# Optimization experiments

Measured on AMD Instinct MI355X. Metric: run time of the kernel, lower is better.

The kernel has to match this reference:

```python
import jax, jax.numpy as jnp
import numpy as np

B, T, C, H = 4, 4096, 1024, 128

def setup_inputs() -> dict:
    key = jax.random.key(0)
    k1, k2, k3, k4 = jax.random.split(key, 4)
    x = jax.random.normal(k1, (B, T, C), dtype=jnp.float32)
    # nn.Linear(embed, head, bias=False): y = x @ W, store W as [C, H]
    s = 1.0 / np.sqrt(C)
    Wk = jax.random.normal(k2, (C, H), dtype=jnp.float32) * s
    Wq = jax.random.normal(k3, (C, H), dtype=jnp.float32) * s
    Wv = jax.random.normal(k4, (C, H), dtype=jnp.float32) * s
    return {"x": x, "Wk": Wk, "Wq": Wq, "Wv": Wv}

def reference(x, Wk, Wq, Wv):
    Bx, Tx, Cx = x.shape
    scale = Wk.shape[1] ** -0.5
    k = x @ Wk  # [B,T,H]
    q = x @ Wq
    v = x @ Wv
    att = jnp.einsum('bth,bsh->bts', q, k) * scale  # [B,T,T]
    causal = jnp.triu(jnp.ones((Tx, Tx), dtype=bool), k=1)
    att = jnp.where(causal, -jnp.inf, att)
    att = jax.nn.softmax(att, axis=-1)
    # dropout is identity in eval mode
    out = jnp.einsum('bts,bsh->bth', att, v)  # [B,T,H]
    return out
```

## Files before the change

### kernel.cpp

```cpp
#include <hip/hip_runtime.h>
#include <stdint.h>
#include <math.h>

#define B_ 4
#define T_ 4096
#define C_ 1024
#define H_ 128

typedef __attribute__((ext_vector_type(8))) short s16x8;
typedef __attribute__((ext_vector_type(4))) float f32x4;

__device__ __forceinline__ unsigned short f2bf(float f) {
    union { float f; unsigned u; } v; v.f = f;
    unsigned r = v.u + 0x7fffu + ((v.u >> 16) & 1u);
    return (unsigned short)(r >> 16);
}

__device__ __forceinline__ s16x8 as_frag(uint4 u) {
    union { uint4 u; s16x8 s; } v; v.u = u; return v.s;
}

#define DPP_STEP(x, ctrl, op)                                                  \
    x = op(x, __int_as_float(__builtin_amdgcn_update_dpp(                      \
               0, __float_as_int(x), ctrl, 0xF, 0xF, true)))

__device__ __forceinline__ float red16_max(float x) {
    DPP_STEP(x, 0xB1, fmaxf); DPP_STEP(x, 0x4E, fmaxf);
    DPP_STEP(x, 0x141, fmaxf); DPP_STEP(x, 0x140, fmaxf);
    return x;
}
__device__ __forceinline__ float addf(float a, float b) { return a + b; }
__device__ __forceinline__ float red16_sum(float x) {
    DPP_STEP(x, 0xB1, addf); DPP_STEP(x, 0x4E, addf);
    DPP_STEP(x, 0x141, addf); DPP_STEP(x, 0x140, addf);
    return x;
}

#define QSC (0.0883883476f * 1.4426950408f)

__global__ __launch_bounds__(256) void k_wt(const float* __restrict__ Wk,
                                            const float* __restrict__ Wq,
                                            const float* __restrict__ Wv,
                                            unsigned short* __restrict__ Wt) {
    __shared__ float tile[64][65];
    int w = blockIdx.z;
    const float* W = (w == 0) ? Wk : (w == 1) ? Wq : Wv;
    int c0 = blockIdx.x * 64, h0 = blockIdx.y * 64;
    int tid = threadIdx.x;
#pragma unroll
    for (int k = 0; k < 16; k++) {
        int idx = tid + k * 256;
        int r = idx >> 6, c = idx & 63;
        tile[r][c] = W[(size_t)(c0 + r) * H_ + h0 + c];
    }
    __syncthreads();
#pragma unroll
    for (int k = 0; k < 16; k++) {
        int idx = tid + k * 256;
        int hh = idx >> 6, cc = idx & 63;
        Wt[(size_t)(w * H_ + h0 + hh) * C_ + c0 + cc] = f2bf(tile[cc][hh]);
    }
}

__global__ __launch_bounds__(256, 2) void k_qkv(const float* __restrict__ x,
                                                const unsigned short* __restrict__ Wt,
                                                unsigned short* __restrict__ Qb,
                                                unsigned short* __restrict__ Kb,
                                                unsigned short* __restrict__ Vt) {
    __shared__ unsigned short a_lds[64 * 72];
    int tid = threadIdx.x;
    int wv = tid >> 6, lane = tid & 63, quad = lane >> 4, lo = lane & 15;
    int r0 = blockIdx.x * 64;
    int cb = blockIdx.y;
    int nt0 = wv * 3;

    f32x4 acc[3][4];
#pragma unroll
    for (int i = 0; i < 3; i++)
#pragma unroll
        for (int j = 0; j < 4; j++) acc[i][j] = (f32x4){0.f, 0.f, 0.f, 0.f};

    const int row_s = tid >> 2;
    const int seg_s = (tid & 3) * 16;
    size_t xbase = (size_t)(r0 + row_s) * C_ + seg_s;

    const unsigned short* wp[3];
#pragma unroll
    for (int nt = 0; nt < 3; nt++)
        wp[nt] = Wt + (size_t)(cb * 192 + (nt0 + nt) * 16 + lo) * C_ + quad * 8;

    auto pack_store = [&](const float4 (&f)[4]) {
        uint4 u0, u1;
        u0.x = (unsigned)f2bf(f[0].x) | ((unsigned)f2bf(f[0].y) << 16);
        u0.y = (unsigned)f2bf(f[0].z) | ((unsigned)f2bf(f[0].w) << 16);
        u0.z = (unsigned)f2bf(f[1].x) | ((unsigned)f2bf(f[1].y) << 16);
        u0.w = (unsigned)f2bf(f[1].z) | ((unsigned)f2bf(f[1].w) << 16);
        u1.x = (unsigned)f2bf(f[2].x) | ((unsigned)f2bf(f[2].y) << 16);
        u1.y = (unsigned)f2bf(f[2].z) | ((unsigned)f2bf(f[2].w) << 16);
        u1.z = (unsigned)f2bf(f[3].x) | ((unsigned)f2bf(f[3].y) << 16);
        u1.w = (unsigned)f2bf(f[3].z) | ((unsigned)f2bf(f[3].w) << 16);
        *(uint4*)&a_lds[row_s * 72 + seg_s] = u0;
        *(uint4*)&a_lds[row_s * 72 + seg_s + 8] = u1;
    };
    auto load_x = [&](float4 (&f)[4], int kc) {
        const float* xp = x + xbase + kc * 64;
#pragma unroll
        for (int j = 0; j < 4; j++) f[j] = *(const float4*)(xp + j * 4);
    };
    auto load_b = [&](s16x8 (&b)[3][2], int kc) {
#pragma unroll
        for (int nt = 0; nt < 3; nt++)
#pragma unroll
            for (int kh = 0; kh < 2; kh++)
                b[nt][kh] = *(const s16x8*)(wp[nt] + kc * 64 + kh * 32);
    };
    auto gemm = [&](const s16x8 (&b)[3][2]) {
        s16x8 af[4][2];
#pragma unroll
        for (int mt = 0; mt < 4; mt++)
#pragma unroll
            for (int kh = 0; kh < 2; kh++)
                af[mt][kh] = *(const s16x8*)&a_lds[(mt * 16 + lo) * 72 + kh * 32 + quad * 8];
#pragma unroll
        for (int nt = 0; nt < 3; nt++)
#pragma unroll
            for (int kh = 0; kh < 2; kh++)
#pragma unroll
                for (int mt = 0; mt < 4; mt++)
                    acc[nt][mt] = __builtin_amdgcn_mfma_f32_16x16x32_bf16(
                        af[mt][kh], b[nt][kh], acc[nt][mt], 0, 0, 0);
    };

    float4 xa[4], xb[4];
    s16x8 ba[3][2], bb[3][2];
    load_x(xa, 0);
    load_b(ba, 0);

    for (int kc2 = 0; kc2 < 8; kc2++) {
        int e = kc2 * 2;
        pack_store(xa);
        load_x(xb, e + 1);
        __syncthreads();
        load_b(bb, e + 1);
        gemm(ba);
        __syncthreads();
        pack_store(xb);
        if (kc2 < 7) load_x(xa, e + 2);
        __syncthreads();
        if (kc2 < 7) load_b(ba, e + 2);
        gemm(bb);
        __syncthreads();
    }

#pragma unroll
    for (int nt = 0; nt < 3; nt++) {
        int col = cb * 192 + (nt0 + nt) * 16 + lo;
        int w = col >> 7, h = col & 127;
#pragma unroll
        for (int mt = 0; mt < 4; mt++) {
            int mrow = r0 + mt * 16 + quad * 4;
            if (w == 2) {
                int b = mrow >> 12, t = mrow & 4095;
                uint2 pk;
                pk.x = (unsigned)f2bf(acc[nt][mt][0]) | ((unsigned)f2bf(acc[nt][mt][1]) << 16);
                pk.y = (unsigned)f2bf(acc[nt][mt][2]) | ((unsigned)f2bf(acc[nt][mt][3]) << 16);
                *(uint2*)(Vt + (size_t)(b * H_ + h) * T_ + t) = pk;
            } else if (w == 1) {
                unsigned short* dst = Qb + (size_t)mrow * H_ + h;
#pragma unroll
                for (int r = 0; r < 4; r++)
                    dst[(size_t)r * H_] = f2bf(acc[nt][mt][r] * QSC);
            } else {
                unsigned short* dst = Kb + (size_t)mrow * H_ + h;
#pragma unroll
                for (int r = 0; r < 4; r++)
                    dst[(size_t)r * H_] = f2bf(acc[nt][mt][r]);
            }
        }
    }
}

#define LOAD_KV(kv0)                                                            \
    do {                                                                        \
        const uint4* kg = (const uint4*)(Kb + (size_t)(batch * T_ + (kv0) + srow_k) * H_); \
        pk0 = kg[sseg_k + 0]; pk1 = kg[sseg_k + 1];                             \
        pk2 = kg[sseg_k + 2]; pk3 = kg[sseg_k + 3];                             \
        const uint4* vg = (const uint4*)(Vt + (size_t)(batch * H_ + srow_v) * T_ + (kv0)); \
        pv0 = vg[sseg_v + 0]; pv1 = vg[sseg_v + 1];                             \
        pv2 = vg[sseg_v + 2]; pv3 = vg[sseg_v + 3];                             \
    } while (0)

template <int NSPLIT>
__global__ __launch_bounds__(256, 3) void k_attn(const unsigned short* __restrict__ Qb,
                                                 const unsigned short* __restrict__ Kb,
                                                 const unsigned short* __restrict__ Vt,
                                                 float* __restrict__ Opart,
                                                 float* __restrict__ Mpart,
                                                 float* __restrict__ Lpart,
                                                 float* __restrict__ out) {
    __shared__ uint4 kbuf[64 * 16];
    __shared__ uint4 vbuf[128 * 8];
    __shared__ unsigned short pbuf[4][16 * 64];

    int tid = threadIdx.x;
    int wv = tid >> 6, lane = tid & 63, quad = lane >> 4, lo = lane & 15;

    int id = blockIdx.x;
    int qt = 63 - id / (4 * NSPLIT);
    int rem = id % (4 * NSPLIT);
    int batch = rem / NSPLIT;
    int split = rem % NSPLIT;
    int m0 = qt * 64 + wv * 16;

    s16x8 qf[4];
    size_t qrow = (size_t)(batch * T_ + m0 + lo) * H_;
#pragma unroll
    for (int ks = 0; ks < 4; ks++)
        qf[ks] = *(const s16x8*)(Qb + qrow + ks * 32 + quad * 8);

    f32x4 acc_o[8];
#pragma unroll
    for (int o = 0; o < 8; o++) acc_o[o] = (f32x4){0.f, 0.f, 0.f, 0.f};
    float m_i[4], l_i[4];
#pragma unroll
    for (int r = 0; r < 4; r++) { m_i[r] = -INFINITY; l_i[r] = 0.f; }

    const int srow_k = tid >> 2, sseg_k = (tid & 3) * 4;
    const int srow_v = tid >> 1, sseg_v = (tid & 1) * 4;

    uint4 pk0, pk1, pk2, pk3, pv0, pv1, pv2, pv3;
    LOAD_KV(split * 64);

    for (int t = split; t <= qt; t += NSPLIT) {
        int kv0 = t * 64;
        kbuf[srow_k * 16 + ((sseg_k + 0) ^ (srow_k & 15))] = pk0;
        kbuf[srow_k * 16 + ((sseg_k + 1) ^ (srow_k & 15))] = pk1;
        kbuf[srow_k * 16 + ((sseg_k + 2) ^ (srow_k & 15))] = pk2;
        kbuf[srow_k * 16 + ((sseg_k + 3) ^ (srow_k & 15))] = pk3;
        vbuf[srow_v * 8 + ((sseg_v + 0) ^ (srow_v & 7))] = pv0;
        vbuf[srow_v * 8 + ((sseg_v + 1) ^ (srow_v & 7))] = pv1;
        vbuf[srow_v * 8 + ((sseg_v + 2) ^ (srow_v & 7))] = pv2;
        vbuf[srow_v * 8 + ((sseg_v + 3) ^ (srow_v & 7))] = pv3;
        __syncthreads();
        if (t + NSPLIT <= qt) LOAD_KV((t + NSPLIT) * 64);

        f32x4 s_acc[4];
#pragma unroll
        for (int nt = 0; nt < 4; nt++) s_acc[nt] = (f32x4){0.f, 0.f, 0.f, 0.f};
#pragma unroll
        for (int ks = 0; ks < 4; ks++) {
#pragma unroll
            for (int nt = 0; nt < 4; nt++) {
                s16x8 kf = as_frag(kbuf[(nt * 16 + lo) * 16 + ((ks * 4 + quad) ^ lo)]);
                s_acc[nt] = __builtin_amdgcn_mfma_f32_16x16x32_bf16(qf[ks], kf, s_acc[nt], 0, 0, 0);
            }
        }

        float p[4][4];
        bool diag = (t == qt);
#pragma unroll
        for (int nt = 0; nt < 4; nt++)
#pragma unroll
            for (int r = 0; r < 4; r++) {
                float sv = s_acc[nt][r];
                if (diag) {
                    int colg = kv0 + nt * 16 + lo;
                    int rowg = m0 + quad * 4 + r;
                    if (colg > rowg) sv = -INFINITY;
                }
                p[nt][r] = sv;
            }
        float mnew[4], alpha[4];
#pragma unroll
        for (int r = 0; r < 4; r++) {
            float mx = fmaxf(fmaxf(p[0][r], p[1][r]), fmaxf(p[2][r], p[3][r]));
            mx = red16_max(mx);
            mnew[r] = fmaxf(m_i[r], mx);
            alpha[r] = exp2f(m_i[r] - mnew[r]);
            m_i[r] = mnew[r];
        }
        float rs[4] = {0.f, 0.f, 0.f, 0.f};
#pragma unroll
        for (int nt = 0; nt < 4; nt++)
#pragma unroll
            for (int r = 0; r < 4; r++) {
                float pv = exp2f(p[nt][r] - mnew[r]);
                p[nt][r] = pv;
                rs[r] += pv;
            }
#pragma unroll
        for (int r = 0; r < 4; r++) {
            l_i[r] = l_i[r] * alpha[r] + red16_sum(rs[r]);
        }
#pragma unroll
        for (int o = 0; o < 8; o++)
#pragma unroll
            for (int r = 0; r < 4; r++) acc_o[o][r] *= alpha[r];

        unsigned short* pb = pbuf[wv];
#pragma unroll
        for (int nt = 0; nt < 4; nt++)
#pragma unroll
            for (int r = 0; r < 4; r++) {
                int prow = quad * 4 + r;
                int col = nt * 16 + lo;
                int seg = col >> 3, off = col & 7;
                pb[prow * 64 + ((seg ^ (prow & 7)) << 3) + off] = f2bf(p[nt][r]);
            }
        s16x8 pf[2];
#pragma unroll
        for (int kss = 0; kss < 2; kss++) {
            int seg = kss * 4 + quad;
            pf[kss] = *(const s16x8*)&pb[lo * 64 + ((seg ^ (lo & 7)) << 3)];
        }

#pragma unroll
        for (int kss = 0; kss < 2; kss++)
#pragma unroll
            for (int o = 0; o < 8; o++) {
                int vrow = o * 16 + lo;
                s16x8 vf = as_frag(vbuf[vrow * 8 + ((kss * 4 + quad) ^ (vrow & 7))]);
                acc_o[o] = __builtin_amdgcn_mfma_f32_16x16x32_bf16(pf[kss], vf, acc_o[o], 0, 0, 0);
            }
        __syncthreads();
    }

    if (NSPLIT == 1) {
        float inv[4];
#pragma unroll
        for (int r = 0; r < 4; r++) inv[r] = 1.0f / l_i[r];
#pragma unroll
        for (int o = 0; o < 8; o++)
#pragma unroll
            for (int r = 0; r < 4; r++) {
                int rowg = batch * T_ + m0 + quad * 4 + r;
                out[(size_t)rowg * H_ + o * 16 + lo] = acc_o[o][r] * inv[r];
            }
    } else {
        float* Op = Opart + (size_t)split * (16384 * 128);
#pragma unroll
        for (int o = 0; o < 8; o++)
#pragma unroll
            for (int r = 0; r < 4; r++) {
                int rowg = batch * T_ + m0 + quad * 4 + r;
                Op[(size_t)rowg * H_ + o * 16 + lo] = acc_o[o][r];
            }
        if (lo == 0) {
#pragma unroll
            for (int r = 0; r < 4; r++) {
                int rowg = batch * T_ + m0 + quad * 4 + r;
                Mpart[split * 16384 + rowg] = m_i[r];
                Lpart[split * 16384 + rowg] = l_i[r];
            }
        }
    }
}

template <int NSPLIT>
__global__ __launch_bounds__(256) void k_comb(const float* __restrict__ Opart,
                                              const float* __restrict__ Mpart,
                                              const float* __restrict__ Lpart,
                                              float* __restrict__ out) {
    int tid = threadIdx.x;
    int row = blockIdx.x * 8 + (tid >> 5);
    int h4 = (tid & 31) * 4;
    float m[NSPLIT], l[NSPLIT];
    float M = -INFINITY;
#pragma unroll
    for (int s = 0; s < NSPLIT; s++) {
        m[s] = Mpart[s * 16384 + row];
        l[s] = Lpart[s * 16384 + row];
        M = fmaxf(M, m[s]);
    }
    float4 o = {0.f, 0.f, 0.f, 0.f};
    float den = 0.f;
#pragma unroll
    for (int s = 0; s < NSPLIT; s++) {
        float w = exp2f(m[s] - M);
        den += w * l[s];
        float4 v = *(const float4*)(Opart + ((size_t)s * 16384 + row) * H_ + h4);
        o.x += w * v.x; o.y += w * v.y; o.z += w * v.z; o.w += w * v.w;
    }
    float inv = 1.0f / den;
    float4 r = {o.x * inv, o.y * inv, o.z * inv, o.w * inv};
    *(float4*)(out + (size_t)row * H_ + h4) = r;
}

extern "C" void kernel_launch(void* const* d_in, const int* in_sizes, int n_in,
                              void* d_out, int out_size, void* d_ws, size_t ws_size,
                              hipStream_t stream) {
    const float* x  = (const float*)d_in[0];
    const float* Wk = (const float*)d_in[1];
    const float* Wq = (const float*)d_in[2];
    const float* Wv = (const float*)d_in[3];
    char* ws = (char*)d_ws;
    unsigned short* Wt = (unsigned short*)ws;
    unsigned short* Qb = (unsigned short*)(ws + (1u << 20));
    unsigned short* Kb = (unsigned short*)(ws + (5u << 20));
    unsigned short* Vt = (unsigned short*)(ws + (9u << 20));
    float* out = (float*)d_out;

    const size_t SPLIT_O = (size_t)16384 * 128 * 4;
    const size_t base = (size_t)13 << 20;
    const size_t need4 = base + 4 * SPLIT_O + 8 * 65536;
    const size_t need2 = base + 2 * SPLIT_O + 4 * 65536;

    k_wt  <<<dim3(16, 2, 3), 256, 0, stream>>>(Wk, Wq, Wv, Wt);
    k_qkv <<<dim3(256, 2), 256, 0, stream>>>(x, Wt, Qb, Kb, Vt);

    if (ws_size >= need4) {
        float* Op = (float*)(ws + base);
        float* Mp = (float*)(ws + base + 4 * SPLIT_O);
        float* Lp = (float*)(ws + base + 4 * SPLIT_O + 4 * 65536);
        k_attn<4><<<1024, 256, 0, stream>>>(Qb, Kb, Vt, Op, Mp, Lp, out);
        k_comb<4><<<2048, 256, 0, stream>>>(Op, Mp, Lp, out);
    } else if (ws_size >= need2) {
        float* Op = (float*)(ws + base);
        float* Mp = (float*)(ws + base + 2 * SPLIT_O);
        float* Lp = (float*)(ws + base + 2 * SPLIT_O + 2 * 65536);
        k_attn<2><<<512, 256, 0, stream>>>(Qb, Kb, Vt, Op, Mp, Lp, out);
        k_comb<2><<<2048, 256, 0, stream>>>(Op, Mp, Lp, out);
    } else {
        k_attn<1><<<256, 256, 0, stream>>>(Qb, Kb, Vt, nullptr, nullptr, nullptr, out);
    }
}
```

Before: 180.1 us.

## Transpose attention MFMA so P stays in registers; double-buffer QKV projection LDS

The attention kernel swaps MFMA operand order so each lane owns one query row. This lets the softmax probabilities be packed straight into bf16 B-fragments instead of round-tripping through shared memory. Row max and sum become two cross-lane shuffles, and rescaling is skipped when no row's max grows. The V layout is permuted to match the new fragment order, the QKV projection moves to a double-buffered LDS loop with higher occupancy, and the output is written as float4. The cost is truncation rounding of P, a tighter register budget, and a more complex V index permutation.

After: 167.6 us. 7.0% less time.

```diff
diff --git a/kernel.cpp b/kernel.cpp
--- a/kernel.cpp
+++ b/kernel.cpp
@@ -18,22 +18,6 @@
 
 __device__ __forceinline__ s16x8 as_frag(uint4 u) {
     union { uint4 u; s16x8 s; } v; v.u = u; return v.s;
-}
-
-#define DPP_STEP(x, ctrl, op)                                                  \
-    x = op(x, __int_as_float(__builtin_amdgcn_update_dpp(                      \
-               0, __float_as_int(x), ctrl, 0xF, 0xF, true)))
-
-__device__ __forceinline__ float red16_max(float x) {
-    DPP_STEP(x, 0xB1, fmaxf); DPP_STEP(x, 0x4E, fmaxf);
-    DPP_STEP(x, 0x141, fmaxf); DPP_STEP(x, 0x140, fmaxf);
-    return x;
-}
-__device__ __forceinline__ float addf(float a, float b) { return a + b; }
-__device__ __forceinline__ float red16_sum(float x) {
-    DPP_STEP(x, 0xB1, addf); DPP_STEP(x, 0x4E, addf);
-    DPP_STEP(x, 0x141, addf); DPP_STEP(x, 0x140, addf);
-    return x;
 }
 
 #define QSC (0.0883883476f * 1.4426950408f)
@@ -62,12 +46,12 @@
     }
 }
 
-__global__ __launch_bounds__(256, 2) void k_qkv(const float* __restrict__ x,
+__global__ __launch_bounds__(256, 3) void k_qkv(const float* __restrict__ x,
                                                 const unsigned short* __restrict__ Wt,
                                                 unsigned short* __restrict__ Qb,
                                                 unsigned short* __restrict__ Kb,
                                                 unsigned short* __restrict__ Vt) {
-    __shared__ unsigned short a_lds[64 * 72];
+    __shared__ unsigned short a_lds[2][64 * 72];
     int tid = threadIdx.x;
     int wv = tid >> 6, lane = tid & 63, quad = lane >> 4, lo = lane & 15;
     int r0 = blockIdx.x * 64;
@@ -89,7 +73,7 @@
     for (int nt = 0; nt < 3; nt++)
         wp[nt] = Wt + (size_t)(cb * 192 + (nt0 + nt) * 16 + lo) * C_ + quad * 8;
 
-    auto pack_store = [&](const float4 (&f)[4]) {
+    auto pack_store = [&](unsigned short* buf, const float4 (&f)[4]) {
         uint4 u0, u1;
         u0.x = (unsigned)f2bf(f[0].x) | ((unsigned)f2bf(f[0].y) << 16);
         u0.y = (unsigned)f2bf(f[0].z) | ((unsigned)f2bf(f[0].w) << 16);
@@ -99,28 +83,36 @@
         u1.y = (unsigned)f2bf(f[2].z) | ((unsigned)f2bf(f[2].w) << 16);
         u1.z = (unsigned)f2bf(f[3].x) | ((unsigned)f2bf(f[3].y) << 16);
         u1.w = (unsigned)f2bf(f[3].z) | ((unsigned)f2bf(f[3].w) << 16);
-        *(uint4*)&a_lds[row_s * 72 + seg_s] = u0;
-        *(uint4*)&a_lds[row_s * 72 + seg_s + 8] = u1;
+        *(uint4*)&buf[row_s * 72 + seg_s] = u0;
+        *(uint4*)&buf[row_s * 72 + seg_s + 8] = u1;
     };
     auto load_x = [&](float4 (&f)[4], int kc) {
         const float* xp = x + xbase + kc * 64;
 #pragma unroll
         for (int j = 0; j < 4; j++) f[j] = *(const float4*)(xp + j * 4);
     };
-    auto load_b = [&](s16x8 (&b)[3][2], int kc) {
+
+    float4 xr[4];
+    load_x(xr, 0);
+    pack_store(a_lds[0], xr);
+    __syncthreads();
+
+    for (int kc = 0; kc < 16; kc++) {
+        const unsigned short* buf = a_lds[kc & 1];
+        float4 xn[4];
+        if (kc < 15) load_x(xn, kc + 1);
+        s16x8 b[3][2];
 #pragma unroll
         for (int nt = 0; nt < 3; nt++)
 #pragma unroll
             for (int kh = 0; kh < 2; kh++)
                 b[nt][kh] = *(const s16x8*)(wp[nt] + kc * 64 + kh * 32);
-    };
-    auto gemm = [&](const s16x8 (&b)[3][2]) {
         s16x8 af[4][2];
 #pragma unroll
         for (int mt = 0; mt < 4; mt++)
 #pragma unroll
             for (int kh = 0; kh < 2; kh++)
-                af[mt][kh] = *(const s16x8*)&a_lds[(mt * 16 + lo) * 72 + kh * 32 + quad * 8];
+                af[mt][kh] = *(const s16x8*)&buf[(mt * 16 + lo) * 72 + kh * 32 + quad * 8];
 #pragma unroll
         for (int nt = 0; nt < 3; nt++)
 #pragma unroll
@@ -129,26 +121,7 @@
                 for (int mt = 0; mt < 4; mt++)
                     acc[nt][mt] = __builtin_amdgcn_mfma_f32_16x16x32_bf16(
                         af[mt][kh], b[nt][kh], acc[nt][mt], 0, 0, 0);
-    };
-
-    float4 xa[4], xb[4];
-    s16x8 ba[3][2], bb[3][2];
-    load_x(xa, 0);
-    load_b(ba, 0);
-
-    for (int kc2 = 0; kc2 < 8; kc2++) {
-        int e = kc2 * 2;
-        pack_store(xa);
-        load_x(xb, e + 1);
-        __syncthreads();
-        load_b(bb, e + 1);
-        gemm(ba);
-        __syncthreads();
-        pack_store(xb);
-        if (kc2 < 7) load_x(xa, e + 2);
-        __syncthreads();
-        if (kc2 < 7) load_b(ba, e + 2);
-        gemm(bb);
+        if (kc < 15) pack_store((unsigned short*)a_lds[(kc & 1) ^ 1], xn);
         __syncthreads();
     }
 
@@ -160,11 +133,12 @@
         for (int mt = 0; mt < 4; mt++) {
             int mrow = r0 + mt * 16 + quad * 4;
             if (w == 2) {
-                int b = mrow >> 12, t = mrow & 4095;
+                int b = mrow >> 12, t0 = mrow & 4095;
+                int tp = (t0 & ~31) + (((t0 & 15) >> 2) << 3) + (((t0 >> 4) & 1) << 2);
                 uint2 pk;
                 pk.x = (unsigned)f2bf(acc[nt][mt][0]) | ((unsigned)f2bf(acc[nt][mt][1]) << 16);
                 pk.y = (unsigned)f2bf(acc[nt][mt][2]) | ((unsigned)f2bf(acc[nt][mt][3]) << 16);
-                *(uint2*)(Vt + (size_t)(b * H_ + h) * T_ + t) = pk;
+                *(uint2*)(Vt + (size_t)(b * H_ + h) * T_ + tp) = pk;
             } else if (w == 1) {
                 unsigned short* dst = Qb + (size_t)mrow * H_ + h;
 #pragma unroll
@@ -200,7 +174,6 @@
                                                  float* __restrict__ out) {
     __shared__ uint4 kbuf[64 * 16];
     __shared__ uint4 vbuf[128 * 8];
-    __shared__ unsigned short pbuf[4][16 * 64];
 
     int tid = threadIdx.x;
     int wv = tid >> 6, lane = tid & 63, quad = lane >> 4, lo = lane & 15;
@@ -211,6 +184,7 @@
     int batch = rem / NSPLIT;
     int split = rem % NSPLIT;
     int m0 = qt * 64 + wv * 16;
+    int query = m0 + lo;
 
     s16x8 qf[4];
     size_t qrow = (size_t)(batch * T_ + m0 + lo) * H_;
@@ -221,15 +195,13 @@
     f32x4 acc_o[8];
 #pragma unroll
     for (int o = 0; o < 8; o++) acc_o[o] = (f32x4){0.f, 0.f, 0.f, 0.f};
-    float m_i[4], l_i[4];
-#pragma unroll
-    for (int r = 0; r < 4; r++) { m_i[r] = -INFINITY; l_i[r] = 0.f; }
+    float m_i = -INFINITY, l_i = 0.f;
 
     const int srow_k = tid >> 2, sseg_k = (tid & 3) * 4;
     const int srow_v = tid >> 1, sseg_v = (tid & 1) * 4;
 
     uint4 pk0, pk1, pk2, pk3, pv0, pv1, pv2, pv3;
-    LOAD_KV(split * 64);
+    if (split <= qt) LOAD_KV(split * 64);
 
     for (int t = split; t <= qt; t += NSPLIT) {
         int kv0 = t * 64;
@@ -252,7 +224,7 @@
 #pragma unroll
             for (int nt = 0; nt < 4; nt++) {
                 s16x8 kf = as_frag(kbuf[(nt * 16 + lo) * 16 + ((ks * 4 + quad) ^ lo)]);
-                s_acc[nt] = __builtin_amdgcn_mfma_f32_16x16x32_bf16(qf[ks], kf, s_acc[nt], 0, 0, 0);
+                s_acc[nt] = __builtin_amdgcn_mfma_f32_16x16x32_bf16(kf, qf[ks], s_acc[nt], 0, 0, 0);
             }
         }
 
@@ -263,95 +235,81 @@
 #pragma unroll
             for (int r = 0; r < 4; r++) {
                 float sv = s_acc[nt][r];
-                if (diag) {
-                    int colg = kv0 + nt * 16 + lo;
-                    int rowg = m0 + quad * 4 + r;
-                    if (colg > rowg) sv = -INFINITY;
-                }
+                if (diag && (kv0 + nt * 16 + quad * 4 + r > query)) sv = -INFINITY;
                 p[nt][r] = sv;
             }
-        float mnew[4], alpha[4];
-#pragma unroll
-        for (int r = 0; r < 4; r++) {
-            float mx = fmaxf(fmaxf(p[0][r], p[1][r]), fmaxf(p[2][r], p[3][r]));
-            mx = red16_max(mx);
-            mnew[r] = fmaxf(m_i[r], mx);
-            alpha[r] = exp2f(m_i[r] - mnew[r]);
-            m_i[r] = mnew[r];
-        }
-        float rs[4] = {0.f, 0.f, 0.f, 0.f};
+
+        float mx = p[0][0];
 #pragma unroll
         for (int nt = 0; nt < 4; nt++)
 #pragma unroll
+            for (int r = 0; r < 4; r++) mx = fmaxf(mx, p[nt][r]);
+        mx = fmaxf(mx, __shfl_xor(mx, 16));
+        mx = fmaxf(mx, __shfl_xor(mx, 32));
+        float mnew = fmaxf(m_i, mx);
+        if (__any(mnew > m_i)) {
+            float alpha = exp2f(m_i - mnew);
+            l_i *= alpha;
+            m_i = mnew;
+#pragma unroll
+            for (int o = 0; o < 8; o++)
+#pragma unroll
+                for (int r = 0; r < 4; r++) acc_o[o][r] *= alpha;
+        }
+        float rs = 0.f;
+#pragma unroll
+        for (int nt = 0; nt < 4; nt++)
+#pragma unroll
             for (int r = 0; r < 4; r++) {
-                float pv = exp2f(p[nt][r] - mnew[r]);
+                float pv = exp2f(p[nt][r] - mnew);
                 p[nt][r] = pv;
-                rs[r] += pv;
-            }
-#pragma unroll
-        for (int r = 0; r < 4; r++) {
-            l_i[r] = l_i[r] * alpha[r] + red16_sum(rs[r]);
-        }
-#pragma unroll
-        for (int o = 0; o < 8; o++)
-#pragma unroll
-            for (int r = 0; r < 4; r++) acc_o[o][r] *= alpha[r];
-
-        unsigned short* pb = pbuf[wv];
-#pragma unroll
-        for (int nt = 0; nt < 4; nt++)
-#pragma unroll
-            for (int r = 0; r < 4; r++) {
-                int prow = quad * 4 + r;
-                int col = nt * 16 + lo;
-                int seg = col >> 3, off = col & 7;
-                pb[prow * 64 + ((seg ^ (prow & 7)) << 3) + off] = f2bf(p[nt][r]);
-            }
+                rs += pv;
+            }
+        rs += __shfl_xor(rs, 16);
+        rs += __shfl_xor(rs, 32);
+        l_i += rs;
+
         s16x8 pf[2];
 #pragma unroll
-        for (int kss = 0; kss < 2; kss++) {
-            int seg = kss * 4 + quad;
-            pf[kss] = *(const s16x8*)&pb[lo * 64 + ((seg ^ (lo & 7)) << 3)];
-        }
-
-#pragma unroll
-        for (int kss = 0; kss < 2; kss++)
+        for (int kt = 0; kt < 2; kt++) {
+            uint4 u;
+            u.x = (__float_as_uint(p[2 * kt][0]) >> 16) | ((__float_as_uint(p[2 * kt][1]) >> 16) << 16);
+            u.y = (__float_as_uint(p[2 * kt][2]) >> 16) | ((__float_as_uint(p[2 * kt][3]) >> 16) << 16);
+            u.z = (__float_as_uint(p[2 * kt + 1][0]) >> 16) | ((__float_as_uint(p[2 * kt + 1][1]) >> 16) << 16);
+            u.w = (__float_as_uint(p[2 * kt + 1][2]) >> 16) | ((__float_as_uint(p[2 * kt + 1][3]) >> 16) << 16);
+            pf[kt] = as_frag(u);
+        }
+
+#pragma unroll
+        for (int kt = 0; kt < 2; kt++)
 #pragma unroll
             for (int o = 0; o < 8; o++) {
                 int vrow = o * 16 + lo;
-                s16x8 vf = as_frag(vbuf[vrow * 8 + ((kss * 4 + quad) ^ (vrow & 7))]);
-                acc_o[o] = __builtin_amdgcn_mfma_f32_16x16x32_bf16(pf[kss], vf, acc_o[o], 0, 0, 0);
+                s16x8 vf = as_frag(vbuf[vrow * 8 + ((kt * 4 + quad) ^ (vrow & 7))]);
+                acc_o[o] = __builtin_amdgcn_mfma_f32_16x16x32_bf16(vf, pf[kt], acc_o[o], 0, 0, 0);
             }
         __syncthreads();
     }
 
+    int rowg = batch * T_ + m0 + lo;
     if (NSPLIT == 1) {
-        float inv[4];
-#pragma unroll
-        for (int r = 0; r < 4; r++) inv[r] = 1.0f / l_i[r];
-#pragma unroll
-        for (int o = 0; o < 8; o++)
-#pragma unroll
-            for (int r = 0; r < 4; r++) {
-                int rowg = batch * T_ + m0 + quad * 4 + r;
-                out[(size_t)rowg * H_ + o * 16 + lo] = acc_o[o][r] * inv[r];
-            }
+        float inv = 1.0f / l_i;
+#pragma unroll
+        for (int o = 0; o < 8; o++) {
+            float4 v = {acc_o[o][0] * inv, acc_o[o][1] * inv,
+                        acc_o[o][2] * inv, acc_o[o][3] * inv};
+            *(float4*)(out + (size_t)rowg * H_ + o * 16 + quad * 4) = v;
+        }
     } else {
         float* Op = Opart + (size_t)split * (16384 * 128);
 #pragma unroll
-        for (int o = 0; o < 8; o++)
-#pragma unroll
-            for (int r = 0; r < 4; r++) {
-                int rowg = batch * T_ + m0 + quad * 4 + r;
-                Op[(size_t)rowg * H_ + o * 16 + lo] = acc_o[o][r];
-            }
-        if (lo == 0) {
-#pragma unroll
-            for (int r = 0; r < 4; r++) {
-                int rowg = batch * T_ + m0 + quad * 4 + r;
-                Mpart[split * 16384 + rowg] = m_i[r];
-                Lpart[split * 16384 + rowg] = l_i[r];
-            }
+        for (int o = 0; o < 8; o++) {
+            float4 v = {acc_o[o][0], acc_o[o][1], acc_o[o][2], acc_o[o][3]};
+            *(float4*)(Op + (size_t)rowg * H_ + o * 16 + quad * 4) = v;
+        }
+        if (quad == 0) {
+            Mpart[split * 16384 + rowg] = m_i;
+            Lpart[split * 16384 + rowg] = l_i;
         }
     }
 }
```
